# Performance work log

Hardware: AMD Instinct MI355X
Metric: run time of the kernel (lower is better)

The kernel has to match this reference:

```python
import jax, jax.numpy as jnp
import numpy as np

B = 131072


def _unfold3(x):
    # torch F.unfold(kernel=3, stride=1, pad=0), feature order (c, kh, kw)
    Bn, C, H, W = x.shape
    Ho, Wo = H - 2, W - 2
    cols = [x[:, :, i:i + Ho, j:j + Wo] for i in range(3) for j in range(3)]
    p = jnp.stack(cols, axis=2)  # (B, C, 9, Ho, Wo)
    return p.reshape(Bn, C * 9, Ho, Wo)


def setup_inputs() -> dict:
    key = jax.random.key(0)
    ks = jax.random.split(key, 7)
    return {
        "x": jax.random.uniform(ks[0], (B, 1, 9, 9), dtype=jnp.float32),
        "w1": jax.random.normal(ks[1], (16, 9), dtype=jnp.float32) * 0.3,
        "b1": jax.random.normal(ks[2], (16,), dtype=jnp.float32) * 0.1,
        "w2": jax.random.normal(ks[3], (32, 144), dtype=jnp.float32) * 0.1,
        "b2": jax.random.normal(ks[4], (32,), dtype=jnp.float32) * 0.1,
        "fc_w": jax.random.normal(ks[5], (4, 32), dtype=jnp.float32) * 0.2,
        "fc_b": jax.random.normal(ks[6], (4,), dtype=jnp.float32) * 0.1,
    }


def reference(x, w1, b1, w2, b2, fc_w, fc_b):
    # LogicConv2d #1: unfold -> per-out-channel optical unit (batched as one einsum)
    p1 = _unfold3(x)  # (B, 9, 7, 7)
    h1 = jax.nn.sigmoid(jnp.einsum('bdhw,od->bohw', p1, w1) + b1[None, :, None, None])
    h1 = jax.nn.relu(h1)
    # MaxPool2d(2,2), floor mode: 7x7 -> 3x3
    h1 = jax.lax.reduce_window(h1, -jnp.inf, jax.lax.max,
                               (1, 1, 2, 2), (1, 1, 2, 2), 'VALID')
    # LogicConv2d #2: 3x3x16 -> 1x1x32
    p2 = _unfold3(h1)  # (B, 144, 1, 1)
    h2 = jax.nn.sigmoid(jnp.einsum('bdhw,od->bohw', p2, w2) + b2[None, :, None, None])
    # flatten + fc
    flat = h2.reshape(h2.shape[0], -1)  # (B, 32)
    return flat @ fc_w.T + fc_b
```

## Files before the change

### kernel.cpp

```cpp
#include <hip/hip_runtime.h>
#include <hip/hip_bf16.h>
#include <math.h>


typedef float v2f __attribute__((ext_vector_type(2)));
typedef float f4  __attribute__((ext_vector_type(4)));
typedef f4 uf4 __attribute__((aligned(4)));
typedef __bf16 bf16x2 __attribute__((ext_vector_type(2)));
typedef __bf16 bf16x8 __attribute__((ext_vector_type(8)));
typedef float f32x16 __attribute__((ext_vector_type(16)));
typedef unsigned int u32;
typedef u32 u32x4 __attribute__((ext_vector_type(4)));

#define BLOCK 256
#define LOG2E 1.4426950408889634f

#define OFF_SMALL 2304
#define S_W1P  0
#define S_B1P  144
#define S_FCWP 160
#define S_B2S  288
#define SMALL_FLOATS 320
#define PREP_ITEMS (4608 + SMALL_FLOATS)

__device__ __forceinline__ float sig2(float s) {
    return __builtin_amdgcn_rcpf(1.0f + __builtin_amdgcn_exp2f(-s));
}

__device__ __forceinline__ u32 pack_bf(float a, float b) {
    bf16x2 p; p.x = (__bf16)a; p.y = (__bf16)b;
    return __builtin_bit_cast(u32, p);
}

__global__ void prep_kernel(const float* __restrict__ w1,
                            const float* __restrict__ b1,
                            const float* __restrict__ w2,
                            const float* __restrict__ b2,
                            const float* __restrict__ fcw,
                            float* __restrict__ ws) {
    int i = blockIdx.x * blockDim.x + threadIdx.x;
    if (i < 4608) {
        int j = i & 7, lane = (i >> 3) & 63, kb = (i >> 9) % 3, pi = i / 1536;
        int k = kb * 16 + (lane >> 5) * 8 + j;
        int o = k / 3, pj = k - 3 * o;
        float v = w2[(lane & 31) * 144 + o * 9 + pi * 3 + pj] * LOG2E;
        ((__bf16*)ws)[i] = (__bf16)v;
    } else if (i < PREP_ITEMS) {
        int r = i - 4608;
        float v;
        if (r < S_B1P) {
            int h = r & 1, k = (r >> 1) % 9, op = (r >> 1) / 9;
            v = w1[(2 * op + h) * 9 + k] * LOG2E;
        } else if (r < S_FCWP) {
            int q = r - S_B1P;
            v = b1[2 * (q >> 1) + (q & 1)] * LOG2E;
        } else if (r < S_B2S) {
            int q = r - S_FCWP;
            int h = q & 1, j = (q >> 1) % 16, rr = (q >> 1) / 16;
            v = fcw[rr * 32 + 2 * j + h];
        } else {
            v = b2[r - S_B2S] * LOG2E;
        }
        ws[OFF_SMALL + r] = v;
    }
}

__global__ __launch_bounds__(BLOCK)
__attribute__((amdgpu_waves_per_eu(2, 2)))
void olcnn_kernel(
    const float* __restrict__ xg,
    const float* __restrict__ wsf,
    const float* __restrict__ fcb,
    float* __restrict__ out)
{
    __shared__ u32 lds_scr[4 * 2176];
    __shared__ __align__(16) float lws[SMALL_FLOATS];

    const int tid  = threadIdx.x;
    const int lane = tid & 63;
    const int wid  = tid >> 6;
    u32* scr = lds_scr + wid * 2176;

    if (tid < SMALL_FLOATS / 4)
        ((f4*)lws)[tid] = ((const f4*)(wsf + OFF_SMALL))[tid];
    __syncthreads();

    const v2f* w1p  = (const v2f*)(lws + S_W1P);
    const v2f* b1p  = (const v2f*)(lws + S_B1P);
    const v2f* fcwp = (const v2f*)(lws + S_FCWP);

    const int t = blockIdx.x * BLOCK + tid;
    const float* xs = xg + (long long)t * 81;

    const u32x4* bfrag_g = (const u32x4*)wsf;

    float xr[8][8];
    #pragma unroll
    for (int r = 0; r < 8; ++r) {
        const float* rp = xs + r * 9;
        f4 a = *(const uf4*)rp;
        f4 b = *(const uf4*)(rp + 4);
        xr[r][0] = a.x; xr[r][1] = a.y; xr[r][2] = a.z; xr[r][3] = a.w;
        xr[r][4] = b.x; xr[r][5] = b.y; xr[r][6] = b.z; xr[r][7] = b.w;
    }
    #pragma unroll
    for (int r = 0; r < 8; ++r)
        #pragma unroll
        for (int c = 0; c < 8; ++c)
            asm volatile("" : "+v"(xr[r][c]));

    f32x16 acc0{};
    f32x16 acc1{};

    const bool h0 = (lane < 32);

    #pragma unroll
    for (int pi = 0; pi < 3; ++pi) {
        u32x4 bfr[3];
        #pragma unroll
        for (int kb = 0; kb < 3; ++kb)
            bfr[kb] = bfrag_g[(pi * 3 + kb) * 64 + lane];

        u32 pk[24];
        #pragma unroll
        for (int op = 0; op < 8; ++op) {
            v2f wv[9];
            #pragma unroll
            for (int k = 0; k < 9; ++k) wv[k] = w1p[op * 9 + k];
            const v2f bb = b1p[op];
            v2f vm[3];
            #pragma unroll
            for (int pj = 0; pj < 3; ++pj) {
                v2f vmax;
                #pragma unroll
                for (int dh = 0; dh < 2; ++dh)
                    #pragma unroll
                    for (int dw = 0; dw < 2; ++dw) {
                        v2f s = bb;
                        #pragma unroll
                        for (int i = 0; i < 3; ++i)
                            #pragma unroll
                            for (int jj = 0; jj < 3; ++jj) {
                                float xv = xr[2 * pi + dh + i][2 * pj + dw + jj];
                                s = __builtin_elementwise_fma(
                                        (v2f){xv, xv}, wv[i * 3 + jj], s);
                            }
                        if (dh == 0 && dw == 0) vmax = s;
                        else vmax = __builtin_elementwise_max(vmax, s);
                    }
                vm[pj] = vmax;
            }
            float s00 = sig2(vm[0].x), s01 = sig2(vm[1].x), s02 = sig2(vm[2].x);
            float s10 = sig2(vm[0].y), s11 = sig2(vm[1].y), s12 = sig2(vm[2].y);
            pk[3 * op + 0] = pack_bf(s00, s01);
            pk[3 * op + 1] = pack_bf(s02, s10);
            pk[3 * op + 2] = pack_bf(s11, s12);
        }

        #pragma unroll
        for (int kb = 0; kb < 3; ++kb) {
            u32 a0d[4], a1d[4];
            #pragma unroll
            for (int i = 0; i < 4; ++i) {
                u32 lo = pk[kb * 8 + i];
                u32 hi = pk[kb * 8 + 4 + i];
                u32 s  = h0 ? hi : lo;
                u32 tt = (u32)__shfl_xor((int)s, 32);
                a0d[i] = h0 ? lo : tt;
                a1d[i] = h0 ? tt : hi;
            }
            u32x4 aw0; aw0.x = a0d[0]; aw0.y = a0d[1]; aw0.z = a0d[2]; aw0.w = a0d[3];
            u32x4 aw1; aw1.x = a1d[0]; aw1.y = a1d[1]; aw1.z = a1d[2]; aw1.w = a1d[3];
            bf16x8 bf = __builtin_bit_cast(bf16x8, bfr[kb]);
            acc0 = __builtin_amdgcn_mfma_f32_32x32x16_bf16(
                       __builtin_bit_cast(bf16x8, aw0), bf, acc0, 0, 0, 0);
            acc1 = __builtin_amdgcn_mfma_f32_32x32x16_bf16(
                       __builtin_bit_cast(bf16x8, aw1), bf, acc1, 0, 0, 0);
        }
    }

    const float b2v = lws[S_B2S + (lane & 31)];
    #pragma unroll
    for (int r = 0; r < 16; ++r) {
        const int srow = (r & 3) + 8 * (r >> 2) + 4 * (lane >> 5);
        scr[srow * 34 + (lane & 31)] =
            __builtin_bit_cast(u32, sig2(acc0[r] + b2v));
        scr[(srow + 32) * 34 + (lane & 31)] =
            __builtin_bit_cast(u32, sig2(acc1[r] + b2v));
    }

    v2f h2[16];
    #pragma unroll
    for (int j = 0; j < 16; ++j)
        h2[j] = *(const v2f*)((const float*)scr + lane * 34 + 2 * j);

    v2f a0 = h2[0] * fcwp[0],  a1 = h2[0] * fcwp[16],
        a2 = h2[0] * fcwp[32], a3 = h2[0] * fcwp[48];
    #pragma unroll
    for (int j = 1; j < 16; ++j) {
        a0 = __builtin_elementwise_fma(h2[j], fcwp[0 * 16 + j], a0);
        a1 = __builtin_elementwise_fma(h2[j], fcwp[1 * 16 + j], a1);
        a2 = __builtin_elementwise_fma(h2[j], fcwp[2 * 16 + j], a2);
        a3 = __builtin_elementwise_fma(h2[j], fcwp[3 * 16 + j], a3);
    }
    ((float4*)out)[t] = make_float4(fcb[0] + a0.x + a0.y,
                                    fcb[1] + a1.x + a1.y,
                                    fcb[2] + a2.x + a2.y,
                                    fcb[3] + a3.x + a3.y);
}

extern "C" void kernel_launch(void* const* d_in, const int* in_sizes, int n_in,
                              void* d_out, int out_size, void* d_ws, size_t ws_size,
                              hipStream_t stream) {
    const float* x   = (const float*)d_in[0];
    const float* w1  = (const float*)d_in[1];
    const float* b1  = (const float*)d_in[2];
    const float* w2  = (const float*)d_in[3];
    const float* b2  = (const float*)d_in[4];
    const float* fcw = (const float*)d_in[5];
    const float* fcb = (const float*)d_in[6];
    float* out = (float*)d_out;
    float* ws  = (float*)d_ws;

    prep_kernel<<<dim3((PREP_ITEMS + 255) / 256), dim3(256), 0, stream>>>(
        w1, b1, w2, b2, fcw, ws);

    const int nB = in_sizes[0] / 81;
    olcnn_kernel<<<dim3(nB / BLOCK), dim3(BLOCK), 0, stream>>>(x, ws, fcb, out);
}
```

Baseline: 131.0 us.

## Stage input tiles through LDS with coalesced loads and roll the pi loop

The block's whole input slab is copied cooperatively into padded LDS with coalesced scalar loads, replacing the per-thread strided 81-float global reads. Each pi iteration then reads only its 4 needed rows from LDS, and the pi loop is no longer unrolled, which should cut live registers that previously held the full 8x8 patch. The LDS buffer is reused as the per-wave scratch for the fc stage. The cost is a large LDS footprint that can limit blocks per CU, plus a serial staging loop with integer division and a block barrier before compute starts.

```diff
diff --git a/kernel.cpp b/kernel.cpp
--- a/kernel.cpp
+++ b/kernel.cpp
@@ -5,7 +5,6 @@
 
 typedef float v2f __attribute__((ext_vector_type(2)));
 typedef float f4  __attribute__((ext_vector_type(4)));
-typedef f4 uf4 __attribute__((aligned(4)));
 typedef __bf16 bf16x2 __attribute__((ext_vector_type(2)));
 typedef __bf16 bf16x8 __attribute__((ext_vector_type(8)));
 typedef float f32x16 __attribute__((ext_vector_type(16)));
@@ -14,6 +13,10 @@
 
 #define BLOCK 256
 #define LOG2E 1.4426950408889634f
+
+#define XSTRIDE 73
+#define XDUMP  (256 * XSTRIDE)
+#define XLDS_FLOATS (256 * XSTRIDE + 64)
 
 #define OFF_SMALL 2304
 #define S_W1P  0
@@ -73,14 +76,24 @@
     const float* __restrict__ fcb,
     float* __restrict__ out)
 {
-    __shared__ u32 lds_scr[4 * 2176];
+    __shared__ float xlds[XLDS_FLOATS];
     __shared__ __align__(16) float lws[SMALL_FLOATS];
 
     const int tid  = threadIdx.x;
     const int lane = tid & 63;
     const int wid  = tid >> 6;
-    u32* scr = lds_scr + wid * 2176;
-
+
+    {
+        const float* xsrc = xg + (long long)blockIdx.x * (BLOCK * 81);
+        #pragma unroll 1
+        for (int i = tid; i < BLOCK * 81; i += BLOCK) {
+            float v = xsrc[i];
+            int s = i / 81;
+            int e = i - s * 81;
+            int addr = (e < 72) ? s * XSTRIDE + e : XDUMP;
+            xlds[addr] = v;
+        }
+    }
     if (tid < SMALL_FLOATS / 4)
         ((f4*)lws)[tid] = ((const f4*)(wsf + OFF_SMALL))[tid];
     __syncthreads();
@@ -90,32 +103,28 @@
     const v2f* fcwp = (const v2f*)(lws + S_FCWP);
 
     const int t = blockIdx.x * BLOCK + tid;
-    const float* xs = xg + (long long)t * 81;
-
     const u32x4* bfrag_g = (const u32x4*)wsf;
-
-    float xr[8][8];
-    #pragma unroll
-    for (int r = 0; r < 8; ++r) {
-        const float* rp = xs + r * 9;
-        f4 a = *(const uf4*)rp;
-        f4 b = *(const uf4*)(rp + 4);
-        xr[r][0] = a.x; xr[r][1] = a.y; xr[r][2] = a.z; xr[r][3] = a.w;
-        xr[r][4] = b.x; xr[r][5] = b.y; xr[r][6] = b.z; xr[r][7] = b.w;
-    }
-    #pragma unroll
-    for (int r = 0; r < 8; ++r)
-        #pragma unroll
-        for (int c = 0; c < 8; ++c)
-            asm volatile("" : "+v"(xr[r][c]));
+    const float* myx = xlds + tid * XSTRIDE;
 
     f32x16 acc0{};
     f32x16 acc1{};
 
     const bool h0 = (lane < 32);
 
-    #pragma unroll
+    #pragma unroll 1
     for (int pi = 0; pi < 3; ++pi) {
+        float xb[4][8];
+        #pragma unroll
+        for (int r = 0; r < 4; ++r)
+            #pragma unroll
+            for (int c = 0; c < 8; ++c)
+                xb[r][c] = myx[(2 * pi + r) * 9 + c];
+        #pragma unroll
+        for (int r = 0; r < 4; ++r)
+            #pragma unroll
+            for (int c = 0; c < 8; ++c)
+                asm volatile("" : "+v"(xb[r][c]));
+
         u32x4 bfr[3];
         #pragma unroll
         for (int kb = 0; kb < 3; ++kb)
@@ -141,7 +150,7 @@
                         for (int i = 0; i < 3; ++i)
                             #pragma unroll
                             for (int jj = 0; jj < 3; ++jj) {
-                                float xv = xr[2 * pi + dh + i][2 * pj + dw + jj];
+                                float xv = xb[dh + i][2 * pj + dw + jj];
                                 s = __builtin_elementwise_fma(
                                         (v2f){xv, xv}, wv[i * 3 + jj], s);
                             }
@@ -179,6 +188,7 @@
         }
     }
 
+    u32* scr = (u32*)(xlds + (wid * 64) * XSTRIDE);
     const float b2v = lws[S_B2S + (lane & 31)];
     #pragma unroll
     for (int r = 0; r < 16; ++r) {
```

Measured after the change: 117.6 us. 10.3% less time.
